# Optimization experiments

Measured on AMD Instinct MI355X. Metric: run time of the kernel, lower is better.

Reference implementation:

```python
import jax, jax.numpy as jnp
import numpy as np


def setup_inputs() -> dict:
    key = jax.random.key(0)
    k0, k1, k2, k3, k4 = jax.random.split(key, 5)
    B, C, H, W, P, M = 8, 128, 256, 256, 32, 2
    return {
        "feats": jax.random.normal(k0, (B, C, H, W), jnp.float32),
        "prototype_centers": jax.random.normal(k1, (P, C), jnp.float32) * 0.01,
        "class_membership": jax.random.uniform(k2, (P, M), jnp.float32),
        "alpha": jax.random.normal(k3, (P, 1), jnp.float32),
        # scaled so gamma^2 * d is O(1) and masses are non-degenerate
        "gamma": jax.random.uniform(k4, (P, 1), jnp.float32) * 0.2,
    }


def reference(feats, prototype_centers, class_membership, alpha, gamma):
    # feats: [B,C,H,W]; prototype_centers: [P,C]; class_membership: [P,M];
    # alpha, gamma: [P,1]. Output: normalized masses [B, M+1, H, W].
    x = feats
    Wp = prototype_centers
    BETA = class_membership
    B, C, H, Wd = x.shape
    P, M = BETA.shape

    BETA2 = BETA * BETA
    U = BETA2 / BETA2.sum(axis=1, keepdims=True)            # [P,M]
    alphap = 0.99 / (1.0 + jnp.exp(-alpha[:, 0]))            # [P]
    g2 = gamma[:, 0] ** 2                                    # [P]

    # d[p,b,h,w] = 0.5 * ||x[b,:,h,w] - W[p,:]||^2, expanded for a GEMM
    xw = jnp.einsum('bchw,pc->pbhw', x, Wp)                  # [P,B,H,W]
    x2 = 0.5 * (x * x).sum(axis=1)                           # [B,H,W]
    w2 = 0.5 * (Wp * Wp).sum(axis=1)                         # [P]
    d = x2[None] - xw + w2[:, None, None, None]              # [P,B,H,W]

    s = alphap[:, None, None, None] * jnp.exp(-g2[:, None, None, None] * d)

    # sequential Dempster-Shafer combination over prototypes (unnormalized)
    def step(carry, inputs):
        cls, om = carry                                      # [M,B,H,W], [B,H,W]
        Uk, sk = inputs                                      # [M], [B,H,W]
        mj = Uk[:, None, None, None] * sk[None]              # class masses of m_k
        mO = 1.0 - sk                                        # omega mass of m_k
        new_cls = cls * mj + cls * mO[None] + mj * om[None]
        new_om = om * mO
        return (new_cls, new_om), None

    init = (jnp.zeros((M, B, H, Wd), x.dtype), jnp.ones((B, H, Wd), x.dtype))
    (cls, om), _ = jax.lax.scan(step, init, (U, s))
    mk = jnp.concatenate([cls, om[None]], axis=0)            # [M+1,B,H,W]
    mk_n = mk / mk.sum(axis=0, keepdims=True)
    return jnp.transpose(mk_n, (1, 0, 2, 3))                 # [B,M+1,H,W]
```

## Files before the change

kernel.cpp:

```cpp
#include <hip/hip_runtime.h>

namespace {
constexpr int C = 128;
constexpr int P = 32;
constexpr int HW = 256 * 256;
constexpr int B = 8;
constexpr int PXW = 32;
constexpr int BLOCK = 256;
constexpr int PIX_PER_BLK = 4 * PXW;
constexpr int BLKS_PER_IMG = HW / PIX_PER_BLK;
constexpr int PREP_BLKS = 8;

typedef __attribute__((ext_vector_type(8))) short short8;
typedef __attribute__((ext_vector_type(4))) float f32x4;

__device__ inline unsigned short f2bf(float f) {
  unsigned u = __builtin_bit_cast(unsigned, f);
  return (unsigned short)((u + 0x7FFFu + ((u >> 16) & 1u)) >> 16);
}
__device__ inline unsigned pack2(float lo, float hi) {
  unsigned r;
  asm("v_cvt_pk_bf16_f32 %0, %1, %2" : "=v"(r) : "v"(lo), "v"(hi));
  return r;
}

__global__ void prep_kernel(const float* __restrict__ Wp,
                            const float* __restrict__ beta,
                            const float* __restrict__ alpha,
                            const float* __restrict__ gam,
                            float* __restrict__ ws) {
  const int t = threadIdx.x;
  if (blockIdx.x == 0) {
    const int p = t >> 3, seg = t & 7;
    float s = 0.f;
#pragma unroll
    for (int i = 0; i < 16; ++i) {
      const float w = Wp[p * C + seg * 16 + i];
      s = fmaf(w, w, s);
    }
#pragma unroll
    for (int m = 1; m < 8; m <<= 1) s += __shfl_xor(s, m);
    if (seg == 0) {
      ws[p] = 0.5f * s;
      ws[32 + p] = 0.99f / (1.f + __expf(-alpha[p]));
      const float gv = gam[p];
      ws[64 + p] = gv * gv;
      const float b0 = beta[p * 2 + 0], b1 = beta[p * 2 + 1];
      const float q0 = b0 * b0, q1 = b1 * b1;
      const float inv = 1.f / (q0 + q1);
      ws[96 + p] = q0 * inv;
      ws[128 + p] = q1 * inv;
    }
  }
  unsigned short* wbf = (unsigned short*)(ws + 160);
  for (int i = blockIdx.x * BLOCK + t; i < P * C; i += PREP_BLKS * BLOCK)
    wbf[i] = f2bf(Wp[i]);
}

__global__ __launch_bounds__(BLOCK) void evid_kernel(const float* __restrict__ x,
                                                     const float* __restrict__ ws,
                                                     float* __restrict__ out) {
  const int t = threadIdx.x;
  const int blk = blockIdx.x;
  const int b = blk >> 9;
  const int px_blk = (blk & (BLKS_PER_IMG - 1)) * PIX_PER_BLK;
  const int wid = t >> 6, l = t & 63;
  const int li = l & 15;
  const int g = l >> 4;
  const int px_wave = px_blk + wid * PXW;
  const float* __restrict__ xg = x + (size_t)b * C * HW + px_wave + 2 * li;
  const unsigned short* __restrict__ wbf = (const unsigned short*)(ws + 160);

  f32x4 acc00 = {0.f, 0.f, 0.f, 0.f};
  f32x4 acc01 = {0.f, 0.f, 0.f, 0.f};
  f32x4 acc10 = {0.f, 0.f, 0.f, 0.f};
  f32x4 acc11 = {0.f, 0.f, 0.f, 0.f};
  float xs0 = 0.f, xs1 = 0.f;
  const int krow0 = g * 8;

#pragma unroll
  for (int s = 0; s < 4; ++s) {
    const float* xr = xg + (size_t)(s * 32 + krow0) * HW;
    float2 v[8];
#pragma unroll
    for (int j = 0; j < 8; ++j)
      v[j] = *reinterpret_cast<const float2*>(xr + (size_t)j * HW);
    union { uint4 q; short8 s8; } a0, a1;
    a0.q = *reinterpret_cast<const uint4*>(wbf + li * C + s * 32 + krow0);
    a1.q = *reinterpret_cast<const uint4*>(wbf + (16 + li) * C + s * 32 + krow0);
    union { unsigned u[4]; short8 s8; } b0, b1;
#pragma unroll
    for (int j = 0; j < 4; ++j) {
      b0.u[j] = pack2(v[2 * j].x, v[2 * j + 1].x);
      b1.u[j] = pack2(v[2 * j].y, v[2 * j + 1].y);
    }
#pragma unroll
    for (int j = 0; j < 8; ++j) {
      xs0 = fmaf(v[j].x, v[j].x, xs0);
      xs1 = fmaf(v[j].y, v[j].y, xs1);
    }
    acc00 = __builtin_amdgcn_mfma_f32_16x16x32_bf16(a0.s8, b0.s8, acc00, 0, 0, 0);
    acc01 = __builtin_amdgcn_mfma_f32_16x16x32_bf16(a1.s8, b0.s8, acc01, 0, 0, 0);
    acc10 = __builtin_amdgcn_mfma_f32_16x16x32_bf16(a0.s8, b1.s8, acc10, 0, 0, 0);
    acc11 = __builtin_amdgcn_mfma_f32_16x16x32_bf16(a1.s8, b1.s8, acc11, 0, 0, 0);
  }

#pragma unroll
  for (int mask = 16; mask <= 32; mask <<= 1) {
    xs0 += __shfl_xor(xs0, mask);
    xs1 += __shfl_xor(xs1, mask);
  }
  const float x2v0 = 0.5f * xs0;
  const float x2v1 = 0.5f * xs1;

  float c00 = 0.f, c01 = 0.f, om0 = 1.f;
  float c10 = 0.f, c11 = 0.f, om1 = 1.f;
#pragma unroll
  for (int r = 0; r < 4; ++r) {
#pragma unroll
    for (int T = 0; T < 2; ++T) {
      const int p = T * 16 + g * 4 + r;
      const float w2h = ws[p];
      const float ap = ws[32 + p];
      const float g2 = ws[64 + p];
      const float U0 = ws[96 + p];
      const float U1 = ws[128 + p];
      const float dot0 = (T == 0) ? acc00[r] : acc01[r];
      const float dot1 = (T == 0) ? acc10[r] : acc11[r];
      {
        const float d = x2v0 + w2h - dot0;
        const float sv = ap * __expf(-g2 * d);
        const float mO = 1.f - sv;
        const float m0 = U0 * sv, m1 = U1 * sv;
        const float n0 = fmaf(c00, m0 + mO, m0 * om0);
        const float n1 = fmaf(c01, m1 + mO, m1 * om0);
        om0 *= mO;
        c00 = n0; c01 = n1;
      }
      {
        const float d = x2v1 + w2h - dot1;
        const float sv = ap * __expf(-g2 * d);
        const float mO = 1.f - sv;
        const float m0 = U0 * sv, m1 = U1 * sv;
        const float n0 = fmaf(c10, m0 + mO, m0 * om1);
        const float n1 = fmaf(c11, m1 + mO, m1 * om1);
        om1 *= mO;
        c10 = n0; c11 = n1;
      }
    }
  }
#pragma unroll
  for (int mask = 16; mask <= 32; mask <<= 1) {
    {
      const float b0 = __shfl_xor(c00, mask);
      const float b1 = __shfl_xor(c01, mask);
      const float bO = __shfl_xor(om0, mask);
      const float n0 = c00 * b0 + c00 * bO + om0 * b0;
      const float n1 = c01 * b1 + c01 * bO + om0 * b1;
      om0 *= bO; c00 = n0; c01 = n1;
    }
    {
      const float b0 = __shfl_xor(c10, mask);
      const float b1 = __shfl_xor(c11, mask);
      const float bO = __shfl_xor(om1, mask);
      const float n0 = c10 * b0 + c10 * bO + om1 * b0;
      const float n1 = c11 * b1 + c11 * bO + om1 * b1;
      om1 *= bO; c10 = n0; c11 = n1;
    }
  }

  if (g == 0) {
    const float inve = __builtin_amdgcn_rcpf(c00 + c01 + om0);
    const float invo = __builtin_amdgcn_rcpf(c10 + c11 + om1);
    float* ob = out + (size_t)b * 3 * HW + px_wave + 2 * li;
    *reinterpret_cast<float2*>(ob) = make_float2(c00 * inve, c10 * invo);
    *reinterpret_cast<float2*>(ob + HW) = make_float2(c01 * inve, c11 * invo);
    *reinterpret_cast<float2*>(ob + 2 * HW) = make_float2(om0 * inve, om1 * invo);
  }
}
}

extern "C" void kernel_launch(void* const* d_in, const int* in_sizes, int n_in,
                              void* d_out, int out_size, void* d_ws, size_t ws_size,
                              hipStream_t stream) {
  const float* feats = (const float*)d_in[0];
  const float* Wp = (const float*)d_in[1];
  const float* beta = (const float*)d_in[2];
  const float* alpha = (const float*)d_in[3];
  const float* gam = (const float*)d_in[4];
  float* ws = (float*)d_ws;
  float* out = (float*)d_out;

  hipLaunchKernelGGL(prep_kernel, dim3(PREP_BLKS), dim3(BLOCK), 0, stream, Wp,
                     beta, alpha, gam, ws);
  hipLaunchKernelGGL(evid_kernel, dim3(B * BLKS_PER_IMG), dim3(BLOCK), 0,
                     stream, feats, ws, out);
}
```

Baseline: 51.25 us.

## Fuse prototype prep into main kernel with padded shared-memory weight tile

```diff
diff --git a/kernel.cpp b/kernel.cpp
--- a/kernel.cpp
+++ b/kernel.cpp
@@ -9,7 +9,7 @@
 constexpr int BLOCK = 256;
 constexpr int PIX_PER_BLK = 4 * PXW;
 constexpr int BLKS_PER_IMG = HW / PIX_PER_BLK;
-constexpr int PREP_BLKS = 8;
+constexpr int WROW = 136;
 
 typedef __attribute__((ext_vector_type(8))) short short8;
 typedef __attribute__((ext_vector_type(4))) float f32x4;
@@ -24,13 +24,16 @@
   return r;
 }
 
-__global__ void prep_kernel(const float* __restrict__ Wp,
-                            const float* __restrict__ beta,
-                            const float* __restrict__ alpha,
-                            const float* __restrict__ gam,
-                            float* __restrict__ ws) {
+__global__ __launch_bounds__(BLOCK) void evid_kernel(
+    const float* __restrict__ x, const float* __restrict__ Wp,
+    const float* __restrict__ beta, const float* __restrict__ alpha,
+    const float* __restrict__ gam, float* __restrict__ out) {
+  __shared__ float tabs[160];
+  __shared__ __align__(16) unsigned short wl[P * WROW];
+
   const int t = threadIdx.x;
-  if (blockIdx.x == 0) {
+
+  {
     const int p = t >> 3, seg = t & 7;
     float s = 0.f;
 #pragma unroll
@@ -41,26 +44,23 @@
 #pragma unroll
     for (int m = 1; m < 8; m <<= 1) s += __shfl_xor(s, m);
     if (seg == 0) {
-      ws[p] = 0.5f * s;
-      ws[32 + p] = 0.99f / (1.f + __expf(-alpha[p]));
+      tabs[p] = 0.5f * s;
+      tabs[32 + p] = 0.99f / (1.f + __expf(-alpha[p]));
       const float gv = gam[p];
-      ws[64 + p] = gv * gv;
+      tabs[64 + p] = gv * gv;
       const float b0 = beta[p * 2 + 0], b1 = beta[p * 2 + 1];
       const float q0 = b0 * b0, q1 = b1 * b1;
       const float inv = 1.f / (q0 + q1);
-      ws[96 + p] = q0 * inv;
-      ws[128 + p] = q1 * inv;
+      tabs[96 + p] = q0 * inv;
+      tabs[128 + p] = q1 * inv;
     }
   }
-  unsigned short* wbf = (unsigned short*)(ws + 160);
-  for (int i = blockIdx.x * BLOCK + t; i < P * C; i += PREP_BLKS * BLOCK)
-    wbf[i] = f2bf(Wp[i]);
-}
+  for (int i = t; i < P * C; i += BLOCK) {
+    const int p = i >> 7, c = i & 127;
+    wl[p * WROW + c] = f2bf(Wp[i]);
+  }
+  __syncthreads();
 
-__global__ __launch_bounds__(BLOCK) void evid_kernel(const float* __restrict__ x,
-                                                     const float* __restrict__ ws,
-                                                     float* __restrict__ out) {
-  const int t = threadIdx.x;
   const int blk = blockIdx.x;
   const int b = blk >> 9;
   const int px_blk = (blk & (BLKS_PER_IMG - 1)) * PIX_PER_BLK;
@@ -69,14 +69,13 @@
   const int g = l >> 4;
   const int px_wave = px_blk + wid * PXW;
   const float* __restrict__ xg = x + (size_t)b * C * HW + px_wave + 2 * li;
-  const unsigned short* __restrict__ wbf = (const unsigned short*)(ws + 160);
+  const int krow0 = g * 8;
 
   f32x4 acc00 = {0.f, 0.f, 0.f, 0.f};
   f32x4 acc01 = {0.f, 0.f, 0.f, 0.f};
   f32x4 acc10 = {0.f, 0.f, 0.f, 0.f};
   f32x4 acc11 = {0.f, 0.f, 0.f, 0.f};
   float xs0 = 0.f, xs1 = 0.f;
-  const int krow0 = g * 8;
 
 #pragma unroll
   for (int s = 0; s < 4; ++s) {
@@ -85,9 +84,9 @@
 #pragma unroll
     for (int j = 0; j < 8; ++j)
       v[j] = *reinterpret_cast<const float2*>(xr + (size_t)j * HW);
-    union { uint4 q; short8 s8; } a0, a1;
-    a0.q = *reinterpret_cast<const uint4*>(wbf + li * C + s * 32 + krow0);
-    a1.q = *reinterpret_cast<const uint4*>(wbf + (16 + li) * C + s * 32 + krow0);
+    union { uint4 q; short8 v8; } a0, a1;
+    a0.q = *reinterpret_cast<const uint4*>(wl + li * WROW + s * 32 + krow0);
+    a1.q = *reinterpret_cast<const uint4*>(wl + (16 + li) * WROW + s * 32 + krow0);
     union { unsigned u[4]; short8 s8; } b0, b1;
 #pragma unroll
     for (int j = 0; j < 4; ++j) {
@@ -99,10 +98,10 @@
       xs0 = fmaf(v[j].x, v[j].x, xs0);
       xs1 = fmaf(v[j].y, v[j].y, xs1);
     }
-    acc00 = __builtin_amdgcn_mfma_f32_16x16x32_bf16(a0.s8, b0.s8, acc00, 0, 0, 0);
-    acc01 = __builtin_amdgcn_mfma_f32_16x16x32_bf16(a1.s8, b0.s8, acc01, 0, 0, 0);
-    acc10 = __builtin_amdgcn_mfma_f32_16x16x32_bf16(a0.s8, b1.s8, acc10, 0, 0, 0);
-    acc11 = __builtin_amdgcn_mfma_f32_16x16x32_bf16(a1.s8, b1.s8, acc11, 0, 0, 0);
+    acc00 = __builtin_amdgcn_mfma_f32_16x16x32_bf16(a0.v8, b0.s8, acc00, 0, 0, 0);
+    acc01 = __builtin_amdgcn_mfma_f32_16x16x32_bf16(a1.v8, b0.s8, acc01, 0, 0, 0);
+    acc10 = __builtin_amdgcn_mfma_f32_16x16x32_bf16(a0.v8, b1.s8, acc10, 0, 0, 0);
+    acc11 = __builtin_amdgcn_mfma_f32_16x16x32_bf16(a1.v8, b1.s8, acc11, 0, 0, 0);
   }
 
 #pragma unroll
@@ -120,11 +119,11 @@
 #pragma unroll
     for (int T = 0; T < 2; ++T) {
       const int p = T * 16 + g * 4 + r;
-      const float w2h = ws[p];
-      const float ap = ws[32 + p];
-      const float g2 = ws[64 + p];
-      const float U0 = ws[96 + p];
-      const float U1 = ws[128 + p];
+      const float w2h = tabs[p];
+      const float ap = tabs[32 + p];
+      const float g2 = tabs[64 + p];
+      const float U0 = tabs[96 + p];
+      const float U1 = tabs[128 + p];
       const float dot0 = (T == 0) ? acc00[r] : acc01[r];
       const float dot1 = (T == 0) ? acc10[r] : acc11[r];
       {
@@ -188,11 +187,8 @@
   const float* beta = (const float*)d_in[2];
   const float* alpha = (const float*)d_in[3];
   const float* gam = (const float*)d_in[4];
-  float* ws = (float*)d_ws;
   float* out = (float*)d_out;
 
-  hipLaunchKernelGGL(prep_kernel, dim3(PREP_BLKS), dim3(BLOCK), 0, stream, Wp,
-                     beta, alpha, gam, ws);
   hipLaunchKernelGGL(evid_kernel, dim3(B * BLKS_PER_IMG), dim3(BLOCK), 0,
-                     stream, feats, ws, out);
+                     stream, feats, Wp, beta, alpha, gam, out);
 }
```

After: 47.44 us. 7.4% less time.
